# Performance work log

Hardware: AMD Instinct MI355X
Metric: run time of the kernel (lower is better)

## Reference

```python
import jax, jax.numpy as jnp
import numpy as np

N = 50000      # nodes
E = 1600000    # edges (avg degree 32)
G = 128        # graphs in batch
NE = 5         # spectral supports (edge_attr channels)
NIN = 16       # input node features
H = 64         # nout1 hidden width
NCLS = 6
BN_EPS = 1e-5


def setup_inputs() -> dict:
    key = jax.random.key(0)
    ks = jax.random.split(key, 12)
    s = 0.1  # weight init scale
    x = jax.random.normal(ks[0], (N, NIN), dtype=jnp.float32)
    edge_index = jax.random.randint(ks[1], (2, E), 0, N, dtype=jnp.int32)
    edge_attr = jax.random.normal(ks[2], (E, NE), dtype=jnp.float32)
    # sorted segment ids covering all G graphs (non-empty segments)
    batch = ((jnp.arange(N, dtype=jnp.int32) * G) // N).astype(jnp.int32)
    W1 = jax.random.normal(ks[3], (NE, NIN, H), dtype=jnp.float32) * s
    W2 = jax.random.normal(ks[4], (NE, H, H), dtype=jnp.float32) * s
    W3 = jax.random.normal(ks[5], (NE, H, H), dtype=jnp.float32) * s
    W4 = jax.random.normal(ks[6], (NE, H, H), dtype=jnp.float32) * s
    b1 = jnp.zeros((H,), jnp.float32)
    b2 = jnp.zeros((H,), jnp.float32)
    b3 = jnp.zeros((H,), jnp.float32)
    b4 = jnp.zeros((H,), jnp.float32)
    bn_gamma = jnp.ones((2 * H,), jnp.float32)
    bn_beta = jnp.zeros((2 * H,), jnp.float32)
    bn_mean = jax.random.normal(ks[7], (2 * H,), dtype=jnp.float32)
    bn_var = jax.random.uniform(ks[8], (2 * H,), dtype=jnp.float32) + 0.5
    fc_w = jax.random.normal(ks[9], (2 * H, NCLS), dtype=jnp.float32) * s
    fc_b = jnp.zeros((NCLS,), jnp.float32)
    return {"x": x, "edge_index": edge_index, "edge_attr": edge_attr,
            "batch": batch, "W1": W1, "b1": b1, "W2": W2, "b2": b2,
            "W3": W3, "b3": b3, "W4": W4, "b4": b4,
            "bn_gamma": bn_gamma, "bn_beta": bn_beta,
            "bn_mean": bn_mean, "bn_var": bn_var,
            "fc_w": fc_w, "fc_b": fc_b}


def spect_conv(x, src, dst, edge_attr, W, b):
    # SpectConv(selfconn=False): out = sum_k scatter_add(edge_attr[:,k]*x[src] -> dst) @ W[k] + b
    xs = x[src]  # [E, F] gather
    n = x.shape[0]
    out = jnp.zeros((n, W.shape[2]), x.dtype)
    for k in range(W.shape[0]):  # K=5 spectral supports
        h = jax.ops.segment_sum(edge_attr[:, k:k + 1] * xs, dst, num_segments=n)
        out = out + h @ W[k]
    return out + b


def reference(x, edge_index, edge_attr, batch, W1, b1, W2, b2, W3, b3, W4, b4,
              bn_gamma, bn_beta, bn_mean, bn_var, fc_w, fc_b):
    src, dst = edge_index[0], edge_index[1]
    h = jax.nn.relu(spect_conv(x, src, dst, edge_attr, W1, b1))
    h = jax.nn.relu(spect_conv(h, src, dst, edge_attr, W2, b2))
    h = jax.nn.relu(spect_conv(h, src, dst, edge_attr, W3, b3))
    h = jax.nn.relu(spect_conv(h, src, dst, edge_attr, W4, b4))
    pooled = jnp.concatenate([
        jax.ops.segment_sum(h, batch, num_segments=G),
        jax.ops.segment_max(h, batch, num_segments=G)], axis=1)  # [G, 2H]
    bn = (pooled - bn_mean) * jax.lax.rsqrt(bn_var + BN_EPS) * bn_gamma + bn_beta
    return jax.nn.log_softmax(bn @ fc_w + fc_b, axis=1)
```

## Files before the change

### kernel.cpp

```cpp
#include <hip/hip_runtime.h>


#define Nn   50000
#define Ne   1600000
#define Gg   128
#define NEk  5
#define NINf 16
#define NCLSo 6
#define NB   196
#define RBK  128
#define CHK  (Ne / RBK)

using short8 = __attribute__((ext_vector_type(8))) short;
using f32x4  = __attribute__((ext_vector_type(4))) float;

__device__ __forceinline__ float2 bf2u(unsigned u) {
    return make_float2(__uint_as_float(u << 16), __uint_as_float(u & 0xffff0000u));
}
__device__ __forceinline__ unsigned f2bf(float a, float b) {
    unsigned ua = __float_as_uint(a), ub = __float_as_uint(b);
    ua += 0x7fffu + ((ua >> 16) & 1u);
    ub += 0x7fffu + ((ub >> 16) & 1u);
    return (ua >> 16) | (ub & 0xffff0000u);
}
__device__ __forceinline__ unsigned short f2bf1(float a) {
    unsigned ua = __float_as_uint(a);
    ua += 0x7fffu + ((ua >> 16) & 1u);
    return (unsigned short)(ua >> 16);
}


__global__ void k_pad_x(const float* __restrict__ x, unsigned* __restrict__ h0) {
    int i = blockIdx.x * 256 + threadIdx.x;
    if (i >= Nn * 32) return;
    int n = i >> 5, p = i & 31;
    int f0 = 2 * p;
    float v0 = (f0 < NINf) ? x[n * NINf + f0] : 0.f;
    float v1 = (f0 + 1 < NINf) ? x[n * NINf + f0 + 1] : 0.f;
    h0[i] = f2bf(v0, v1);
}

__global__ void k_pad_w1(const float* __restrict__ W1, float* __restrict__ W1p) {
    int i = blockIdx.x * 256 + threadIdx.x;
    if (i >= NEk * 64 * 64) return;
    int h = i & 63, f = (i >> 6) & 63, k = i >> 12;
    W1p[i] = (f < NINf) ? W1[(k * NINf + f) * 64 + h] : 0.f;
}

__global__ void k_pack_b(const float* __restrict__ W, unsigned short* __restrict__ bhi,
                         unsigned short* __restrict__ blo) {
    int i = blockIdx.x * 256 + threadIdx.x;
    if (i >= 20480) return;
    int j = i & 7, lane = (i >> 3) & 63, t2 = i >> 9;
    int nt = t2 / 10, kstep = t2 - nt * 10;
    int k = kstep * 32 + (lane >> 4) * 8 + j;
    int col = nt * 16 + (lane & 15);
    float v = W[k * 64 + col];
    unsigned short hi = f2bf1(v);
    float fhi = __uint_as_float(((unsigned)hi) << 16);
    bhi[i] = hi;
    blo[i] = f2bf1(v - fhi);
}

__global__ __launch_bounds__(1024) void k_rankhist(
    const int* __restrict__ ei, unsigned short* __restrict__ lrank,
    unsigned short* __restrict__ cnt ) {
    __shared__ unsigned hist[12500];
    int b = blockIdx.x, t = threadIdx.x;
    int e0 = b * CHK;
#pragma unroll 1
    for (int h = 0; h < 2; ++h) {
        int lo = h * 25000;
        for (int w = t; w < 12500; w += 1024) hist[w] = 0;
        __syncthreads();
        for (int i = t; i < CHK; i += 1024) {
            int d = ei[Ne + e0 + i];
            unsigned dd = (unsigned)(d - lo);
            if (dd < 25000u) {
                unsigned old = atomicAdd(&hist[dd >> 1], (dd & 1u) ? 65536u : 1u);
                lrank[e0 + i] = (unsigned short)(old >> (16 * (dd & 1u)));
            }
        }
        __syncthreads();
        unsigned* co = (unsigned*)(cnt + (size_t)b * Nn + lo);
        for (int w = t; w < 12500; w += 1024) co[w] = hist[w];
        __syncthreads();
    }
}

__global__ void k_colscan(unsigned short* __restrict__ cnt, int* __restrict__ deg) {
    int d = blockIdx.x * 256 + threadIdx.x;
    if (d >= Nn) return;
    int s = 0;
#pragma unroll 4
    for (int b = 0; b < RBK; ++b) {
        int t = cnt[(size_t)b * Nn + d];
        cnt[(size_t)b * Nn + d] = (unsigned short)s;
        s += t;
    }
    deg[d] = s;
}


__global__ void k_blocksum(const int* __restrict__ deg, int* __restrict__ bsum) {
    __shared__ int l[256];
    int t = threadIdx.x;
    int i = blockIdx.x * 256 + t;
    l[t] = (i < Nn) ? deg[i] : 0;
    __syncthreads();
    for (int off = 128; off > 0; off >>= 1) {
        if (t < off) l[t] += l[t + off];
        __syncthreads();
    }
    if (t == 0) bsum[blockIdx.x] = l[0];
}

__global__ void k_scanpart(const int* __restrict__ bsum, int* __restrict__ boff) {
    __shared__ int l[256];
    int t = threadIdx.x;
    int v = (t < NB) ? bsum[t] : 0;
    l[t] = v;
    __syncthreads();
    for (int off = 1; off < 256; off <<= 1) {
        int u = (t >= off) ? l[t - off] : 0;
        __syncthreads();
        l[t] += u;
        __syncthreads();
    }
    if (t < NB) boff[t] = l[t] - v;
}

__global__ void k_scanfinal(const int* __restrict__ deg, const int* __restrict__ boff,
                            int* __restrict__ rowstart) {
    __shared__ int l[256];
    int t = threadIdx.x;
    int i = blockIdx.x * 256 + t;
    int v = (i < Nn) ? deg[i] : 0;
    l[t] = v;
    __syncthreads();
    for (int off = 1; off < 256; off <<= 1) {
        int u = (t >= off) ? l[t - off] : 0;
        __syncthreads();
        l[t] += u;
        __syncthreads();
    }
    if (i <= Nn) rowstart[i] = boff[blockIdx.x] + l[t] - v;
}

__global__ void k_place(const int* __restrict__ ei, const float* __restrict__ eattr,
                        const int* __restrict__ rowstart,
                        const unsigned short* __restrict__ lrank,
                        const unsigned short* __restrict__ cnt,
                        uint4* __restrict__ recs) {
    int e = blockIdx.x * 256 + threadIdx.x;
    if (e >= Ne) return;
    int d = ei[Ne + e];
    int b = e / CHK;
    int pos = rowstart[d] + cnt[(size_t)b * Nn + d] + lrank[e];
    const float* a = eattr + (size_t)e * 5;
    uint4 rr;
    rr.x = (unsigned)ei[e];
    rr.y = f2bf(a[0], a[1]);
    rr.z = f2bf(a[2], a[3]);
    rr.w = f2bf(a[4], 0.f);
    recs[pos] = rr;
}

__global__ void k_bounds(const int* __restrict__ batch, int* __restrict__ sg,
                         int* __restrict__ eg) {
    int n = blockIdx.x * 256 + threadIdx.x;
    if (n >= Nn) return;
    int g = batch[n];
    if (n == 0) sg[g] = 0;
    else {
        int gp = batch[n - 1];
        if (gp != g) { sg[g] = n; eg[gp] = n; }
    }
    if (n == Nn - 1) eg[g] = Nn;
}


__global__ __launch_bounds__(256) void k_aggregate(
    const unsigned* __restrict__ hin, const int* __restrict__ rowstart,
    const uint4* __restrict__ recs, unsigned* __restrict__ agg) {
    int lane = threadIdx.x & 63;
    int l = lane & 31, half = lane >> 5;
    int node = __builtin_amdgcn_readfirstlane((int)(blockIdx.x * 4 + (threadIdx.x >> 6)));
    int beg = rowstart[node], end = rowstart[node + 1];
    float2 c0 = {0.f, 0.f}, c1 = c0, c2 = c0, c3 = c0, c4 = c0;
    int ee = beg;
#define EDGE(E) { \
    uint4 r = recs[(E)]; \
    unsigned hx = hin[(size_t)(int)r.x * 32 + l]; \
    float2 xv = bf2u(hx); \
    float2 A01 = bf2u(r.y), A23 = bf2u(r.z); \
    float a4v = __uint_as_float(r.w << 16); \
    c0.x = fmaf(A01.x, xv.x, c0.x); c0.y = fmaf(A01.x, xv.y, c0.y); \
    c1.x = fmaf(A01.y, xv.x, c1.x); c1.y = fmaf(A01.y, xv.y, c1.y); \
    c2.x = fmaf(A23.x, xv.x, c2.x); c2.y = fmaf(A23.x, xv.y, c2.y); \
    c3.x = fmaf(A23.y, xv.x, c3.x); c3.y = fmaf(A23.y, xv.y, c3.y); \
    c4.x = fmaf(a4v,  xv.x, c4.x); c4.y = fmaf(a4v,  xv.y, c4.y); }
    for (; ee + 8 <= end; ee += 8) {
        EDGE(ee + half) EDGE(ee + 2 + half) EDGE(ee + 4 + half) EDGE(ee + 6 + half)
    }
    for (; ee + 2 <= end; ee += 2) { EDGE(ee + half) }
    if (ee < end) { if (half == 0) { EDGE(ee) } }
#undef EDGE
    c0.x += __shfl(c0.x, lane ^ 32); c0.y += __shfl(c0.y, lane ^ 32);
    c1.x += __shfl(c1.x, lane ^ 32); c1.y += __shfl(c1.y, lane ^ 32);
    c2.x += __shfl(c2.x, lane ^ 32); c2.y += __shfl(c2.y, lane ^ 32);
    c3.x += __shfl(c3.x, lane ^ 32); c3.y += __shfl(c3.y, lane ^ 32);
    c4.x += __shfl(c4.x, lane ^ 32); c4.y += __shfl(c4.y, lane ^ 32);
    if (half == 0) {
        unsigned* o = agg + (size_t)node * 160 + l;
        o[0]   = f2bf(c0.x, c0.y);
        o[32]  = f2bf(c1.x, c1.y);
        o[64]  = f2bf(c2.x, c2.y);
        o[96]  = f2bf(c3.x, c3.y);
        o[128] = f2bf(c4.x, c4.y);
    }
}

#define SPAD 41
__global__ __launch_bounds__(256) void k_transform(
    const uint4* __restrict__ A, const unsigned short* __restrict__ bhi,
    const unsigned short* __restrict__ blo, const float* __restrict__ bias,
    unsigned* __restrict__ outh) {
    __shared__ uint4 smem[64 * SPAD];
    int t = threadIdx.x;
    int lane = t & 63, wave = t >> 6;
    int m = lane & 15, quad = lane >> 4;
    int blk = blockIdx.x;

#pragma unroll
    for (int it = 0; it < 10; ++it) {
        int v = t + it * 256;
        int row = v / 40, off = v - row * 40;
        int node = blk * 64 + row;
        if (node >= Nn) node = Nn - 1;
        smem[row * SPAD + off] = A[(size_t)node * 40 + off];
    }
    __syncthreads();

    f32x4 acc0 = {0.f, 0.f, 0.f, 0.f}, acc1 = acc0, acc2 = acc0, acc3 = acc0;
    const uint4* arow = smem + (wave * 16 + m) * SPAD + quad;
#pragma unroll 2
    for (int ks = 0; ks < 10; ++ks) {
        short8 a = *(const short8*)(arow + ks * 4);
        size_t bb = ((size_t)ks * 64 + lane) * 8;
        short8 h0 = *(const short8*)(bhi + bb);
        short8 l0 = *(const short8*)(blo + bb);
        acc0 = __builtin_amdgcn_mfma_f32_16x16x32_bf16(a, h0, acc0, 0, 0, 0);
        acc0 = __builtin_amdgcn_mfma_f32_16x16x32_bf16(a, l0, acc0, 0, 0, 0);
        short8 h1 = *(const short8*)(bhi + bb + 5120);
        short8 l1 = *(const short8*)(blo + bb + 5120);
        acc1 = __builtin_amdgcn_mfma_f32_16x16x32_bf16(a, h1, acc1, 0, 0, 0);
        acc1 = __builtin_amdgcn_mfma_f32_16x16x32_bf16(a, l1, acc1, 0, 0, 0);
        short8 h2 = *(const short8*)(bhi + bb + 10240);
        short8 l2 = *(const short8*)(blo + bb + 10240);
        acc2 = __builtin_amdgcn_mfma_f32_16x16x32_bf16(a, h2, acc2, 0, 0, 0);
        acc2 = __builtin_amdgcn_mfma_f32_16x16x32_bf16(a, l2, acc2, 0, 0, 0);
        short8 h3 = *(const short8*)(bhi + bb + 15360);
        short8 l3 = *(const short8*)(blo + bb + 15360);
        acc3 = __builtin_amdgcn_mfma_f32_16x16x32_bf16(a, h3, acc3, 0, 0, 0);
        acc3 = __builtin_amdgcn_mfma_f32_16x16x32_bf16(a, l3, acc3, 0, 0, 0);
    }
    __syncthreads();

    float* Cs = (float*)smem;
#pragma unroll
    for (int r = 0; r < 4; ++r) {
        int base = wave * 1152 + (quad * 4 + r) * 72 + m;
        Cs[base]      = acc0[r];
        Cs[base + 16] = acc1[r];
        Cs[base + 32] = acc2[r];
        Cs[base + 48] = acc3[r];
    }
    __syncthreads();

    int row = t >> 2, grp = t & 3;
    int node = blk * 64 + row;
    if (node < Nn) {
        const float* cr = Cs + (row >> 4) * 1152 + (row & 15) * 72;
        unsigned o[8];
#pragma unroll
        for (int j = 0; j < 8; ++j) {
            int pp = grp * 8 + j;
            float v0 = fmaxf(cr[2 * pp]     + bias[2 * pp],     0.f);
            float v1 = fmaxf(cr[2 * pp + 1] + bias[2 * pp + 1], 0.f);
            o[j] = f2bf(v0, v1);
        }
        uint4* dst = (uint4*)(outh + (size_t)node * 32 + grp * 8);
        dst[0] = make_uint4(o[0], o[1], o[2], o[3]);
        dst[1] = make_uint4(o[4], o[5], o[6], o[7]);
    }
}


__global__ __launch_bounds__(256) void k_pool(const unsigned* __restrict__ h,
                                              const int* __restrict__ sg,
                                              const int* __restrict__ eg,
                                              float* __restrict__ pooled) {
    __shared__ float2 ls[256], lm[256];
    int g = blockIdx.x, t = threadIdx.x;
    int p = t & 31, q = t >> 5;
    int s = sg[g], e = eg[g];
    float2 sum = {0.f, 0.f}, mx = {0.f, 0.f};
    for (int n = s + q; n < e; n += 8) {
        float2 v = bf2u(h[(size_t)n * 32 + p]);
        sum.x += v.x; sum.y += v.y;
        mx.x = fmaxf(mx.x, v.x); mx.y = fmaxf(mx.y, v.y);
    }
    ls[t] = sum; lm[t] = mx;
    __syncthreads();
    if (t < 32) {
        float2 ss = ls[t], mm = lm[t];
        for (int i = 1; i < 8; ++i) {
            float2 a = ls[t + i * 32], b = lm[t + i * 32];
            ss.x += a.x; ss.y += a.y;
            mm.x = fmaxf(mm.x, b.x); mm.y = fmaxf(mm.y, b.y);
        }
        pooled[g * 128 + 2 * t]          = ss.x;
        pooled[g * 128 + 2 * t + 1]      = ss.y;
        pooled[g * 128 + 64 + 2 * t]     = mm.x;
        pooled[g * 128 + 64 + 2 * t + 1] = mm.y;
    }
}

__global__ void k_head(const float* __restrict__ pooled, const float* __restrict__ gamma,
                       const float* __restrict__ beta, const float* __restrict__ mean,
                       const float* __restrict__ var, const float* __restrict__ fcw,
                       const float* __restrict__ fcb, float* __restrict__ out) {
    __shared__ float y[128];
    __shared__ float lg[8];
    int g = blockIdx.x, c = threadIdx.x;
    float p = pooled[g * 128 + c];
    y[c] = (p - mean[c]) * rsqrtf(var[c] + 1e-5f) * gamma[c] + beta[c];
    __syncthreads();
    if (c < NCLSo) {
        float l = fcb[c];
        for (int i = 0; i < 128; ++i) l += y[i] * fcw[i * NCLSo + c];
        lg[c] = l;
    }
    __syncthreads();
    if (c == 0) {
        float m = lg[0];
        for (int j = 1; j < NCLSo; ++j) m = fmaxf(m, lg[j]);
        float se = 0.f;
        for (int j = 0; j < NCLSo; ++j) se += expf(lg[j] - m);
        float lse = m + logf(se);
        for (int j = 0; j < NCLSo; ++j) out[g * NCLSo + j] = lg[j] - lse;
    }
}


static inline size_t rup(size_t x) { return (x + 255) & ~(size_t)255; }

extern "C" void kernel_launch(void* const* d_in, const int* in_sizes, int n_in,
                              void* d_out, int out_size, void* d_ws, size_t ws_size,
                              hipStream_t stream) {
    const float* x     = (const float*)d_in[0];
    const int*   ei    = (const int*)d_in[1];
    const float* eattr = (const float*)d_in[2];
    const int*   batch = (const int*)d_in[3];
    const float* W1    = (const float*)d_in[4];
    const float* b1    = (const float*)d_in[5];
    const float* W2    = (const float*)d_in[6];
    const float* b2    = (const float*)d_in[7];
    const float* W3    = (const float*)d_in[8];
    const float* b3    = (const float*)d_in[9];
    const float* W4    = (const float*)d_in[10];
    const float* b4    = (const float*)d_in[11];
    const float* gamma = (const float*)d_in[12];
    const float* beta  = (const float*)d_in[13];
    const float* mean  = (const float*)d_in[14];
    const float* var   = (const float*)d_in[15];
    const float* fcw   = (const float*)d_in[16];
    const float* fcb   = (const float*)d_in[17];
    float* out = (float*)d_out;

    char* p = (char*)d_ws;
    auto take = [&](size_t bytes) { char* r = p; p += rup(bytes); return r; };
    int*            deg      = (int*)take((size_t)(Nn + 1) * 4);
    unsigned short* cnt      = (unsigned short*)take((size_t)RBK * Nn * 2);
    unsigned short* lrank    = (unsigned short*)take((size_t)Ne * 2);
    int*            rowstart = (int*)take((size_t)(Nn + 1) * 4);
    int*            bsum     = (int*)take((size_t)NB * 4);
    int*            boff     = (int*)take((size_t)NB * 4);
    uint4*          recs     = (uint4*)take((size_t)Ne * 16);
    unsigned*       hA       = (unsigned*)take((size_t)Nn * 32 * 4);
    unsigned*       hB       = (unsigned*)take((size_t)Nn * 32 * 4);
    unsigned*       agg      = (unsigned*)take((size_t)Nn * 160 * 4);
    float*          W1p      = (float*)take((size_t)NEk * 64 * 64 * 4);
    unsigned short* bhiA     = (unsigned short*)take((size_t)4 * 20480 * 2);
    unsigned short* bloA     = (unsigned short*)take((size_t)4 * 20480 * 2);
    float*          pooled   = (float*)take((size_t)Gg * 128 * 4);
    int*            sg       = (int*)take((size_t)Gg * 4);
    int*            eg       = (int*)take((size_t)Gg * 4);

    k_rankhist<<<RBK, 1024, 0, stream>>>(ei, lrank, cnt);
    k_pad_x<<<(Nn * 32 + 255) / 256, 256, 0, stream>>>(x, hA);
    k_pad_w1<<<(NEk * 64 * 64 + 255) / 256, 256, 0, stream>>>(W1, W1p);
    k_pack_b<<<80, 256, 0, stream>>>(W1p, bhiA,             bloA);
    k_pack_b<<<80, 256, 0, stream>>>(W2,  bhiA + 20480,     bloA + 20480);
    k_pack_b<<<80, 256, 0, stream>>>(W3,  bhiA + 2 * 20480, bloA + 2 * 20480);
    k_pack_b<<<80, 256, 0, stream>>>(W4,  bhiA + 3 * 20480, bloA + 3 * 20480);
    k_colscan<<<NB, 256, 0, stream>>>(cnt, deg);
    k_blocksum<<<NB, 256, 0, stream>>>(deg, bsum);
    k_scanpart<<<1, 256, 0, stream>>>(bsum, boff);
    k_scanfinal<<<NB, 256, 0, stream>>>(deg, boff, rowstart);
    k_place<<<(Ne + 255) / 256, 256, 0, stream>>>(ei, eattr, rowstart, lrank, cnt, recs);
    k_bounds<<<(Nn + 255) / 256, 256, 0, stream>>>(batch, sg, eg);

    const float* bs[4] = { b1, b2, b3, b4 };
    unsigned* cur = hA;
    unsigned* nxt = hB;
    for (int L = 0; L < 4; ++L) {
        k_aggregate<<<Nn / 4, 256, 0, stream>>>(cur, rowstart, recs, agg);
        k_transform<<<(Nn + 63) / 64, 256, 0, stream>>>(
            (const uint4*)agg, bhiA + (size_t)L * 20480, bloA + (size_t)L * 20480,
            bs[L], nxt);
        unsigned* tmp = cur; cur = nxt; nxt = tmp;
    }

    k_pool<<<Gg, 256, 0, stream>>>(cur, sg, eg, pooled);
    k_head<<<Gg, 128, 0, stream>>>(pooled, gamma, beta, mean, var, fcw, fcb, out);
}
```

Before: 479.0 us.

## Fuse edge aggregation and MFMA transform into one per-layer kernel

Merges the aggregate and transform kernels into a single 512-thread kernel per layer. Each wave aggregates 8 nodes into shared memory, then the 8 waves split the 64x64 MFMA output by row and column halves. This removes the global round trip of the bf16 aggregation buffer (about 32 MB written and read per layer) and one launch per layer. The trade-off is fewer, larger blocks: 782 blocks where each wave works through nodes serially, and more shared memory per block, which may reduce latency hiding for the irregular gathers.

Result: slower. 564.5 us (+17.8%).

```diff
diff --git a/kernel.cpp b/kernel.cpp
--- a/kernel.cpp
+++ b/kernel.cpp
@@ -179,16 +179,28 @@
     if (n == Nn - 1) eg[g] = Nn;
 }
 
-
-__global__ __launch_bounds__(256) void k_aggregate(
+#define SPAD 41
+__global__ __launch_bounds__(512) void k_layer(
     const unsigned* __restrict__ hin, const int* __restrict__ rowstart,
-    const uint4* __restrict__ recs, unsigned* __restrict__ agg) {
-    int lane = threadIdx.x & 63;
+    const uint4* __restrict__ recs, const unsigned short* __restrict__ bhi,
+    const unsigned short* __restrict__ blo, const float* __restrict__ bias,
+    unsigned* __restrict__ outh) {
+    __shared__ uint4 smem[64 * SPAD];
+    unsigned* aggw = (unsigned*)smem;
+    int t = threadIdx.x;
+    int lane = t & 63, wave = t >> 6;
     int l = lane & 31, half = lane >> 5;
-    int node = __builtin_amdgcn_readfirstlane((int)(blockIdx.x * 4 + (threadIdx.x >> 6)));
-    int beg = rowstart[node], end = rowstart[node + 1];
-    float2 c0 = {0.f, 0.f}, c1 = c0, c2 = c0, c3 = c0, c4 = c0;
-    int ee = beg;
+    int blk = blockIdx.x;
+
+#pragma unroll 1
+    for (int ni = 0; ni < 8; ++ni) {
+        int row = wave * 8 + ni;
+        int node = blk * 64 + row;
+        if (node >= Nn) node = Nn - 1;
+        node = __builtin_amdgcn_readfirstlane(node);
+        int beg = rowstart[node], end = rowstart[node + 1];
+        float2 c0 = {0.f, 0.f}, c1 = c0, c2 = c0, c3 = c0, c4 = c0;
+        int ee = beg;
 #define EDGE(E) { \
     uint4 r = recs[(E)]; \
     unsigned hx = hin[(size_t)(int)r.x * 32 + l]; \
@@ -200,54 +212,37 @@
     c2.x = fmaf(A23.x, xv.x, c2.x); c2.y = fmaf(A23.x, xv.y, c2.y); \
     c3.x = fmaf(A23.y, xv.x, c3.x); c3.y = fmaf(A23.y, xv.y, c3.y); \
     c4.x = fmaf(a4v,  xv.x, c4.x); c4.y = fmaf(a4v,  xv.y, c4.y); }
-    for (; ee + 8 <= end; ee += 8) {
-        EDGE(ee + half) EDGE(ee + 2 + half) EDGE(ee + 4 + half) EDGE(ee + 6 + half)
-    }
-    for (; ee + 2 <= end; ee += 2) { EDGE(ee + half) }
-    if (ee < end) { if (half == 0) { EDGE(ee) } }
+        for (; ee + 8 <= end; ee += 8) {
+            EDGE(ee + half) EDGE(ee + 2 + half) EDGE(ee + 4 + half) EDGE(ee + 6 + half)
+        }
+        for (; ee + 2 <= end; ee += 2) { EDGE(ee + half) }
+        if (ee < end) { if (half == 0) { EDGE(ee) } }
 #undef EDGE
-    c0.x += __shfl(c0.x, lane ^ 32); c0.y += __shfl(c0.y, lane ^ 32);
-    c1.x += __shfl(c1.x, lane ^ 32); c1.y += __shfl(c1.y, lane ^ 32);
-    c2.x += __shfl(c2.x, lane ^ 32); c2.y += __shfl(c2.y, lane ^ 32);
-    c3.x += __shfl(c3.x, lane ^ 32); c3.y += __shfl(c3.y, lane ^ 32);
-    c4.x += __shfl(c4.x, lane ^ 32); c4.y += __shfl(c4.y, lane ^ 32);
-    if (half == 0) {
-        unsigned* o = agg + (size_t)node * 160 + l;
-        o[0]   = f2bf(c0.x, c0.y);
-        o[32]  = f2bf(c1.x, c1.y);
-        o[64]  = f2bf(c2.x, c2.y);
-        o[96]  = f2bf(c3.x, c3.y);
-        o[128] = f2bf(c4.x, c4.y);
-    }
-}
-
-#define SPAD 41
-__global__ __launch_bounds__(256) void k_transform(
-    const uint4* __restrict__ A, const unsigned short* __restrict__ bhi,
-    const unsigned short* __restrict__ blo, const float* __restrict__ bias,
-    unsigned* __restrict__ outh) {
-    __shared__ uint4 smem[64 * SPAD];
-    int t = threadIdx.x;
-    int lane = t & 63, wave = t >> 6;
+        c0.x += __shfl(c0.x, lane ^ 32); c0.y += __shfl(c0.y, lane ^ 32);
+        c1.x += __shfl(c1.x, lane ^ 32); c1.y += __shfl(c1.y, lane ^ 32);
+        c2.x += __shfl(c2.x, lane ^ 32); c2.y += __shfl(c2.y, lane ^ 32);
+        c3.x += __shfl(c3.x, lane ^ 32); c3.y += __shfl(c3.y, lane ^ 32);
+        c4.x += __shfl(c4.x, lane ^ 32); c4.y += __shfl(c4.y, lane ^ 32);
+        if (half == 0) {
+            unsigned* o = aggw + row * (SPAD * 4) + l;
+            o[0]   = f2bf(c0.x, c0.y);
+            o[32]  = f2bf(c1.x, c1.y);
+            o[64]  = f2bf(c2.x, c2.y);
+            o[96]  = f2bf(c3.x, c3.y);
+            o[128] = f2bf(c4.x, c4.y);
+        }
+    }
+    __syncthreads();
+
     int m = lane & 15, quad = lane >> 4;
-    int blk = blockIdx.x;
-
-#pragma unroll
-    for (int it = 0; it < 10; ++it) {
-        int v = t + it * 256;
-        int row = v / 40, off = v - row * 40;
-        int node = blk * 64 + row;
-        if (node >= Nn) node = Nn - 1;
-        smem[row * SPAD + off] = A[(size_t)node * 40 + off];
-    }
-    __syncthreads();
-
-    f32x4 acc0 = {0.f, 0.f, 0.f, 0.f}, acc1 = acc0, acc2 = acc0, acc3 = acc0;
-    const uint4* arow = smem + (wave * 16 + m) * SPAD + quad;
+    int wr = wave >> 1, wc = wave & 1;
+    f32x4 acc0 = {0.f, 0.f, 0.f, 0.f}, acc1 = acc0;
+    const uint4* arow = smem + (wr * 16 + m) * SPAD + quad;
+    const size_t boff = (size_t)(wc * 2) * 5120;
 #pragma unroll 2
     for (int ks = 0; ks < 10; ++ks) {
         short8 a = *(const short8*)(arow + ks * 4);
-        size_t bb = ((size_t)ks * 64 + lane) * 8;
+        size_t bb = ((size_t)ks * 64 + lane) * 8 + boff;
         short8 h0 = *(const short8*)(bhi + bb);
         short8 l0 = *(const short8*)(blo + bb);
         acc0 = __builtin_amdgcn_mfma_f32_16x16x32_bf16(a, h0, acc0, 0, 0, 0);
@@ -256,43 +251,35 @@
         short8 l1 = *(const short8*)(blo + bb + 5120);
         acc1 = __builtin_amdgcn_mfma_f32_16x16x32_bf16(a, h1, acc1, 0, 0, 0);
         acc1 = __builtin_amdgcn_mfma_f32_16x16x32_bf16(a, l1, acc1, 0, 0, 0);
-        short8 h2 = *(const short8*)(bhi + bb + 10240);
-        short8 l2 = *(const short8*)(blo + bb + 10240);
-        acc2 = __builtin_amdgcn_mfma_f32_16x16x32_bf16(a, h2, acc2, 0, 0, 0);
-        acc2 = __builtin_amdgcn_mfma_f32_16x16x32_bf16(a, l2, acc2, 0, 0, 0);
-        short8 h3 = *(const short8*)(bhi + bb + 15360);
-        short8 l3 = *(const short8*)(blo + bb + 15360);
-        acc3 = __builtin_amdgcn_mfma_f32_16x16x32_bf16(a, h3, acc3, 0, 0, 0);
-        acc3 = __builtin_amdgcn_mfma_f32_16x16x32_bf16(a, l3, acc3, 0, 0, 0);
     }
     __syncthreads();
 
     float* Cs = (float*)smem;
 #pragma unroll
     for (int r = 0; r < 4; ++r) {
-        int base = wave * 1152 + (quad * 4 + r) * 72 + m;
+        int base = wr * 1152 + (quad * 4 + r) * 72 + wc * 32 + m;
         Cs[base]      = acc0[r];
         Cs[base + 16] = acc1[r];
-        Cs[base + 32] = acc2[r];
-        Cs[base + 48] = acc3[r];
-    }
-    __syncthreads();
-
-    int row = t >> 2, grp = t & 3;
-    int node = blk * 64 + row;
-    if (node < Nn) {
-        const float* cr = Cs + (row >> 4) * 1152 + (row & 15) * 72;
-        unsigned o[8];
+    }
+    __syncthreads();
+
+    if (t < 256) {
+        int row = t >> 2, grp = t & 3;
+        int node = blk * 64 + row;
+        if (node < Nn) {
+            const float* cr = Cs + (row >> 4) * 1152 + (row & 15) * 72;
+            unsigned o[8];
 #pragma unroll
-        for (int j = 0; j < 8; ++j) {
-            int pp = grp * 8 + j;
-            float v0 = fmaxf(cr[2 * pp]     + bias[2 * pp],     0.f);
-            float v1 = fmaxf(cr[2 * pp + 1] + bias[2 * pp + 1], 0.f);
-            o[j] = f2bf(v0, v1);
+            for (int j = 0; j < 8; ++j) {
+                int pp = grp * 8 + j;
+                float v0 = fmaxf(cr[2 * pp]     + bias[2 * pp],     0.f);
+                float v1 = fmaxf(cr[2 * pp + 1] + bias[2 * pp + 1], 0.f);
+                o[j] = f2bf(v0, v1);
+            }
+            uint4* dst = (uint4*)(outh + (size_t)node * 32 + grp * 8);
+            dst[0] = make_uint4(o[0], o[1], o[2], o[3]);
+            dst[1] = make_uint4(o[4], o[5], o[6], o[7]);
         }
-        uint4* dst = (uint4*)(outh + (size_t)node * 32 + grp * 8);
-        dst[0] = make_uint4(o[0], o[1], o[2], o[3]);
-        dst[1] = make_uint4(o[4], o[5], o[6], o[7]);
     }
 }
 
@@ -390,7 +377,6 @@
     uint4*          recs     = (uint4*)take((size_t)Ne * 16);
     unsigned*       hA       = (unsigned*)take((size_t)Nn * 32 * 4);
     unsigned*       hB       = (unsigned*)take((size_t)Nn * 32 * 4);
-    unsigned*       agg      = (unsigned*)take((size_t)Nn * 160 * 4);
     float*          W1p      = (float*)take((size_t)NEk * 64 * 64 * 4);
     unsigned short* bhiA     = (unsigned short*)take((size_t)4 * 20480 * 2);
     unsigned short* bloA     = (unsigned short*)take((size_t)4 * 20480 * 2);
@@ -416,9 +402,8 @@
     unsigned* cur = hA;
     unsigned* nxt = hB;
     for (int L = 0; L < 4; ++L) {
-        k_aggregate<<<Nn / 4, 256, 0, stream>>>(cur, rowstart, recs, agg);
-        k_transform<<<(Nn + 63) / 64, 256, 0, stream>>>(
-            (const uint4*)agg, bhiA + (size_t)L * 20480, bloA + (size_t)L * 20480,
+        k_layer<<<(Nn + 63) / 64, 512, 0, stream>>>(
+            cur, rowstart, recs, bhiA + (size_t)L * 20480, bloA + (size_t)L * 20480,
             bs[L], nxt);
         unsigned* tmp = cur; cur = nxt; nxt = tmp;
     }
```
